# Performance work log

Hardware: AMD Instinct MI355X
Metric: run time of the kernel (lower is better)

Reference implementation:

```python
import jax, jax.numpy as jnp
import numpy as np


def setup_inputs() -> dict:
    key = jax.random.key(0)
    ks = jax.random.split(key, 5)
    B, N, D = 8, 2048, 512
    return {
        "query": jax.random.normal(ks[0], (B, N, D), dtype=jnp.float32),
        "key": jax.random.normal(ks[1], (B, N, D), dtype=jnp.float32),
        "value": jax.random.normal(ks[2], (B, N, D), dtype=jnp.float32),
        "w_k": jax.random.normal(ks[3], (2 * N - 1, D), dtype=jnp.float32),
        "w_v": jax.random.normal(ks[4], (2 * N - 1, D), dtype=jnp.float32),
    }


def reference(query, key, value, w_k, w_v):
    B, N, D = query.shape
    # skew indices: idx[i, j] = (N-1) - i + j  maps (i,j) -> relative distance j-i,
    # distance 0 sits at the middle column (N-1) of the 2N-1 relative table.
    idx = (N - 1) - jnp.arange(N)[:, None] + jnp.arange(N)[None, :]  # [N, N]

    # content scores: [B, N, N]
    base_scores = jnp.einsum("bqd,bkd->bqk", query, key)
    # relative key scores: matmul against full 2N-1 table then skewed gather
    all_rel = jnp.einsum("bqd,rd->bqr", query, w_k)  # [B, N, 2N-1]
    rel_scores = jnp.take_along_axis(
        all_rel, jnp.broadcast_to(idx[None], (B, N, N)), axis=-1
    )
    p_attn = jax.nn.softmax(base_scores + rel_scores, axis=-1)  # [B, N, N]

    # value path: scatter probabilities into skewed [B, N, 2N-1] layout,
    # then one matmul against the relative value table (equivalent to
    # sum_j p[i,j] * w_v[(N-1)-i+j]).
    rows = jnp.arange(N)[:, None]  # [N, 1] broadcast against idx [N, N]
    p_skew = jnp.zeros((B, N, 2 * N - 1), dtype=p_attn.dtype)
    p_skew = p_skew.at[:, rows, idx].set(p_attn)
    rel_out = jnp.einsum("bqr,rd->bqd", p_skew, w_v)

    out = jnp.einsum("bqk,bkd->bqd", p_attn, value) + rel_out
    return out, p_attn
```

## Files before the change

### kernel.cpp

```cpp
#include <hip/hip_runtime.h>


#define SEQN 2048
#define DD   512
#define NB   8
#define WROWS 4095
#define WPAD  4096

typedef float     f32x4 __attribute__((ext_vector_type(4)));
typedef _Float16  h16x4 __attribute__((ext_vector_type(4)));
typedef _Float16  h16x8 __attribute__((ext_vector_type(8)));

__device__ __forceinline__ unsigned swzw(int row, int c4) {
  unsigned b = (unsigned)(row * 64 + c4 * 8);
  return b ^ (((unsigned)row & 6u) << 3);
}
__device__ __forceinline__ unsigned swzr(int row, int kg) {
  unsigned b = (unsigned)(row * 64 + kg * 16);
  return b ^ (((unsigned)row & 6u) << 3);
}

typedef const __attribute__((address_space(1))) unsigned int gu32_t;
typedef __attribute__((address_space(3))) unsigned int lu32_t;
__device__ __forceinline__ void gload_lds16(const void* g, void* l) {
  __builtin_amdgcn_global_load_lds((gu32_t*)g, (lu32_t*)l, 16, 0, 0);
}

template <class P>
__device__ __forceinline__ void stage_tile(const P& prov, char* smem, int buf,
                                           int t, int wave, int l4, int cp) {
  char* lb = smem + buf * 16384;
#pragma unroll
  for (int h = 0; h < 2; h++) {
    int R = wave * 32 + h * 16;
    int row = R + l4;
    int c = cp ^ ((row >> 1) & 3);
    gload_lds16((const char*)prov.a_src(t, row) + c * 16, lb + R * 64);
    gload_lds16((const char*)prov.b_src(t, row) + c * 16, lb + 8192 + R * 64);
  }
}

template <int NT, class P>
__device__ __forceinline__ void gemm_core(const P& prov, char* smem, f32x4 (&acc)[4][4]) {
  const int tid = threadIdx.x;
  const int lane = tid & 63, wave = tid >> 6;
  const int l4 = lane >> 2, cp = lane & 3;
  const int wm = wave >> 1, wn = wave & 1;
  const int r16 = lane & 15, kg = lane >> 4;

  stage_tile(prov, smem, 0, 0, wave, l4, cp);
  asm volatile("s_waitcnt vmcnt(0)" ::: "memory");
  __builtin_amdgcn_s_barrier();
  __builtin_amdgcn_sched_barrier(0);

  int buf = 0;
  for (int t = 0; t < NT; t++) {
    if (t + 1 < NT) stage_tile(prov, smem, buf ^ 1, t + 1, wave, l4, cp);
    char* lb = smem + buf * 16384;
    h16x8 af[4], bf[4];
#pragma unroll
    for (int mf = 0; mf < 4; mf++)
      af[mf] = *(const h16x8*)(lb + swzr(wm * 64 + mf * 16 + r16, kg));
#pragma unroll
    for (int nf = 0; nf < 4; nf++)
      bf[nf] = *(const h16x8*)(lb + 8192 + swzr(wn * 64 + nf * 16 + r16, kg));
#pragma unroll
    for (int mf = 0; mf < 4; mf++)
#pragma unroll
      for (int nf = 0; nf < 4; nf++)
        acc[mf][nf] = __builtin_amdgcn_mfma_f32_16x16x32_f16(af[mf], bf[nf], acc[mf][nf], 0, 0, 0);
    asm volatile("s_waitcnt vmcnt(0)" ::: "memory");
    __builtin_amdgcn_s_barrier();
    __builtin_amdgcn_sched_barrier(0);
    buf ^= 1;
  }
}

struct ProvQK {
  const char *ar, *br;
  __device__ __forceinline__ const void* a_src(int t, int row) const {
    return ar + (size_t)row * 1024 + (size_t)t * 64;
  }
  __device__ __forceinline__ const void* b_src(int t, int row) const {
    return br + (size_t)row * 1024 + (size_t)t * 64;
  }
};
struct ProvRel {
  const char *ar, *wk; int tb;
  __device__ __forceinline__ const void* a_src(int t, int row) const {
    return ar + (size_t)row * 1024 + (size_t)t * 64;
  }
  __device__ __forceinline__ const void* b_src(int t, int row) const {
    int tr = tb + row; if (tr > WROWS - 1) tr = WROWS - 1;
    return wk + (size_t)tr * 1024 + (size_t)t * 64;
  }
};

__global__ __launch_bounds__(256) void cvt_f16_k(const float* __restrict__ in,
                                                 _Float16* __restrict__ out, long n8) {
  for (long i = (long)blockIdx.x * 256 + threadIdx.x; i < n8; i += (long)gridDim.x * 256) {
    f32x4 a = ((const f32x4*)in)[i * 2];
    f32x4 b = ((const f32x4*)in)[i * 2 + 1];
    h16x8 h = {(_Float16)a[0], (_Float16)a[1], (_Float16)a[2], (_Float16)a[3],
               (_Float16)b[0], (_Float16)b[1], (_Float16)b[2], (_Float16)b[3]};
    ((h16x8*)out)[i] = h;
  }
}

__global__ __launch_bounds__(256) void transpose_v_k(const float* __restrict__ v,
                                                     _Float16* __restrict__ vT) {
  __shared__ float tile[32][33];
  const int d0 = blockIdx.x * 32, j0 = blockIdx.y * 32, b = blockIdx.z;
  const int tid = threadIdx.x;
#pragma unroll
  for (int rep = 0; rep < 4; rep++) {
    int idx = rep * 256 + tid;
    int rr = idx >> 5, cc = idx & 31;
    tile[rr][cc] = v[((size_t)(b * SEQN + j0 + rr)) * DD + d0 + cc];
  }
  __syncthreads();
#pragma unroll
  for (int rep = 0; rep < 4; rep++) {
    int idx = rep * 256 + tid;
    int rr = idx >> 5, cc = idx & 31;
    vT[((size_t)(b * DD + d0 + rr)) * SEQN + j0 + cc] = (_Float16)tile[cc][rr];
  }
}

__global__ __launch_bounds__(256) void transpose_wv_k(const float* __restrict__ wv,
                                                      _Float16* __restrict__ wvT) {
  __shared__ float tile[32][33];
  const int d0 = blockIdx.x * 32, r0 = blockIdx.y * 32;
  const int tid = threadIdx.x;
#pragma unroll
  for (int rep = 0; rep < 4; rep++) {
    int idx = rep * 256 + tid;
    int rr = idx >> 5, cc = idx & 31;
    float val = 0.f;
    if (r0 + rr < WROWS) val = wv[(size_t)(r0 + rr) * DD + d0 + cc];
    tile[rr][cc] = val;
  }
  __syncthreads();
#pragma unroll
  for (int rep = 0; rep < 4; rep++) {
    int idx = rep * 256 + tid;
    int rr = idx >> 5, cc = idx & 31;
    wvT[(size_t)(d0 + rr) * WPAD + r0 + cc] = (_Float16)tile[cc][rr];
  }
}

__global__ __launch_bounds__(256) void score_base2_k(const _Float16* __restrict__ qh,
                                                     const _Float16* __restrict__ kh,
                                                     float* __restrict__ S) {
  __shared__ __align__(16) char smem[32768];
  const int j0 = blockIdx.x * 128, i0 = blockIdx.y * 128, b = blockIdx.z;
  const int tid = threadIdx.x, lane = tid & 63, wave = tid >> 6;
  const int wm = wave >> 1, wn = wave & 1, r16 = lane & 15, kg = lane >> 4;

  f32x4 acc[4][4];
#pragma unroll
  for (int mf = 0; mf < 4; mf++)
#pragma unroll
    for (int nf = 0; nf < 4; nf++) acc[mf][nf] = (f32x4){0.f, 0.f, 0.f, 0.f};

  ProvQK prov{(const char*)(qh + (size_t)(b * SEQN + i0) * DD),
              (const char*)(kh + (size_t)(b * SEQN + j0) * DD)};
  gemm_core<16>(prov, smem, acc);

#pragma unroll
  for (int mf = 0; mf < 4; mf++)
#pragma unroll
    for (int nf = 0; nf < 4; nf++)
#pragma unroll
      for (int r = 0; r < 4; r++) {
        int ii = wm * 64 + mf * 16 + kg * 4 + r;
        int jj = wn * 64 + nf * 16 + r16;
        S[(size_t)(b * SEQN + i0 + ii) * SEQN + j0 + jj] = acc[mf][nf][r];
      }
}

__global__ __launch_bounds__(256) void score_rel2_k(const _Float16* __restrict__ qh,
                                                    const _Float16* __restrict__ wkh,
                                                    float* __restrict__ S) {
  __shared__ __align__(16) char smem[32768];
  const int z = blockIdx.x, i0 = blockIdx.y * 128, b = blockIdx.z;
  const int tid = threadIdx.x, lane = tid & 63, wave = tid >> 6;
  const int wm = wave >> 1, wn = wave & 1, r16 = lane & 15, kg = lane >> 4;
  const int tmin = SEQN - 128 - i0;

  f32x4 acc[4][4];
#pragma unroll
  for (int mf = 0; mf < 4; mf++)
#pragma unroll
    for (int nf = 0; nf < 4; nf++) acc[mf][nf] = (f32x4){0.f, 0.f, 0.f, 0.f};

  ProvRel prov{(const char*)(qh + (size_t)(b * SEQN + i0) * DD),
               (const char*)wkh, tmin + z * 128};
  gemm_core<16>(prov, smem, acc);

#pragma unroll
  for (int mf = 0; mf < 4; mf++)
#pragma unroll
    for (int nf = 0; nf < 4; nf++) {
      int bcg = z * 128 + wn * 64 + nf * 16 + r16;
#pragma unroll
      for (int r = 0; r < 4; r++) {
        int ii = wm * 64 + mf * 16 + kg * 4 + r;
        int j = bcg + ii - 127;
        if (bcg <= 2174 && j >= 0 && j < SEQN)
          S[(size_t)(b * SEQN + i0 + ii) * SEQN + j] += acc[mf][nf][r];
      }
    }
}

__global__ __launch_bounds__(256) void softmax_rows_k(float* __restrict__ S) {
  const int wid = threadIdx.x >> 6, lane = threadIdx.x & 63;
  const size_t row = (size_t)blockIdx.x * 4 + wid;
  float* p = S + row * SEQN;
  f32x4 x[8];
  float m = -3.4e38f;
#pragma unroll
  for (int c = 0; c < 8; c++) {
    x[c] = *(const f32x4*)(p + c * 256 + lane * 4);
    m = fmaxf(m, fmaxf(fmaxf(x[c][0], x[c][1]), fmaxf(x[c][2], x[c][3])));
  }
#pragma unroll
  for (int off = 32; off > 0; off >>= 1) m = fmaxf(m, __shfl_xor(m, off));
  float s = 0.f;
#pragma unroll
  for (int c = 0; c < 8; c++)
#pragma unroll
    for (int e = 0; e < 4; e++) {
      x[c][e] = __expf(x[c][e] - m);
      s += x[c][e];
    }
#pragma unroll
  for (int off = 32; off > 0; off >>= 1) s += __shfl_xor(s, off);
  float inv = 1.f / s;
#pragma unroll
  for (int c = 0; c < 8; c++) {
    x[c][0] *= inv; x[c][1] *= inv; x[c][2] *= inv; x[c][3] *= inv;
    *(f32x4*)(p + c * 256 + lane * 4) = x[c];
  }
}

__global__ __launch_bounds__(256) void out_gemm3_k(const float* __restrict__ S,
                                                   const _Float16* __restrict__ vT,
                                                   const _Float16* __restrict__ wvT,
                                                   float* __restrict__ outp) {
  __shared__ __align__(16) char smem[32768];
  const int bid = blockIdx.x;
  const int xcd = bid & 7, rr = bid >> 3;
  const int x = rr & 3, s8 = rr >> 2;
  const int sidx = xcd + 8 * s8;
  const int d0 = x * 128, i0 = (sidx & 15) * 128, b = sidx >> 4;
  const int tid = threadIdx.x, lane = tid & 63, wave = tid >> 6;
  const int wm = wave >> 1, wn = wave & 1, r16 = lane & 15, kg = lane >> 4;
  const int tmin = SEQN - 128 - i0;

  const float*    pb = S  + (size_t)(b * SEQN + i0) * SEQN;
  const _Float16* vb = vT + (size_t)(b * DD + d0) * SEQN;
  const _Float16* wb = wvT + (size_t)d0 * WPAD + tmin;

  f32x4 acc[4][4];
#pragma unroll
  for (int mf = 0; mf < 4; mf++)
#pragma unroll
    for (int nf = 0; nf < 4; nf++) acc[mf][nf] = (f32x4){0.f, 0.f, 0.f, 0.f};

  f32x4 ra[4];
  h16x4 rbv[4];

  auto LOADREGS = [&](int t) {
    if (t < 64) {
      const int k0 = t * 32;
#pragma unroll
      for (int rep = 0; rep < 4; rep++) {
        int f = rep * 256 + tid, row = f >> 3, c4 = f & 7;
        ra[rep]  = *(const f32x4*)(pb + (size_t)row * SEQN + k0 + c4 * 4);
        rbv[rep] = *(const h16x4*)(vb + (size_t)row * SEQN + k0 + c4 * 4);
      }
    } else {
      const int k0 = (t - 64) * 32;
#pragma unroll
      for (int rep = 0; rep < 4; rep++) {
        int f = rep * 256 + tid, row = f >> 3, c4 = f & 7;
        int jb = k0 + c4 * 4 + row - 127;
        const float* pr = pb + (size_t)row * SEQN;
        f32x4 v4;
#pragma unroll
        for (int e = 0; e < 4; e++) {
          int j = jb + e;
          v4[e] = (j >= 0 && j < SEQN) ? pr[j] : 0.f;
        }
        ra[rep]  = v4;
        rbv[rep] = *(const h16x4*)(wb + (size_t)row * WPAD + k0 + c4 * 4);
      }
    }
  };
  auto WRITE = [&](char* lb) {
#pragma unroll
    for (int rep = 0; rep < 4; rep++) {
      int f = rep * 256 + tid, row = f >> 3, c4 = f & 7;
      h16x4 ha = {(_Float16)ra[rep][0], (_Float16)ra[rep][1],
                  (_Float16)ra[rep][2], (_Float16)ra[rep][3]};
      *(h16x4*)(lb + swzw(row, c4)) = ha;
      *(h16x4*)(lb + 8192 + swzw(row, c4)) = rbv[rep];
    }
  };

  LOADREGS(0);
  WRITE(smem);
  LOADREGS(1);
  __syncthreads();

  for (int t = 0; t < 132; t++) {
    char* lb = smem + (t & 1) * 16384;
    if (t + 1 < 132) WRITE(smem + ((t + 1) & 1) * 16384);
    h16x8 af[4], bf[4];
#pragma unroll
    for (int mf = 0; mf < 4; mf++)
      af[mf] = *(const h16x8*)(lb + swzr(wm * 64 + mf * 16 + r16, kg));
#pragma unroll
    for (int nf = 0; nf < 4; nf++)
      bf[nf] = *(const h16x8*)(lb + 8192 + swzr(wn * 64 + nf * 16 + r16, kg));
    if (t + 2 < 132) LOADREGS(t + 2);
#pragma unroll
    for (int mf = 0; mf < 4; mf++)
#pragma unroll
      for (int nf = 0; nf < 4; nf++)
        acc[mf][nf] = __builtin_amdgcn_mfma_f32_16x16x32_f16(af[mf], bf[nf], acc[mf][nf], 0, 0, 0);
    __syncthreads();
  }

#pragma unroll
  for (int mf = 0; mf < 4; mf++)
#pragma unroll
    for (int nf = 0; nf < 4; nf++)
#pragma unroll
      for (int r = 0; r < 4; r++) {
        int ii = wm * 64 + mf * 16 + kg * 4 + r;
        int dd = wn * 64 + nf * 16 + r16;
        outp[(size_t)(b * SEQN + i0 + ii) * DD + d0 + dd] = acc[mf][nf][r];
      }
}

extern "C" void kernel_launch(void* const* d_in, const int* in_sizes, int n_in,
                              void* d_out, int out_size, void* d_ws, size_t ws_size,
                              hipStream_t stream) {
  const float* q  = (const float*)d_in[0];
  const float* k  = (const float*)d_in[1];
  const float* v  = (const float*)d_in[2];
  const float* wk = (const float*)d_in[3];
  const float* wv = (const float*)d_in[4];

  float* outp = (float*)d_out;
  float* S    = outp + (size_t)NB * SEQN * DD;

  const size_t nVT = (size_t)NB * DD * SEQN;
  const size_t nWV = (size_t)DD * WPAD;
  const size_t nQH = (size_t)NB * SEQN * DD;
  _Float16* vT  = (_Float16*)d_ws;
  _Float16* wvT = vT + nVT;
  _Float16* qh  = wvT + nWV;
  _Float16* kh  = qh + nQH;
  _Float16* wkh = kh + nQH;

  cvt_f16_k<<<dim3(2048), 256, 0, stream>>>(q,  qh,  (long)(nQH / 8));
  cvt_f16_k<<<dim3(2048), 256, 0, stream>>>(k,  kh,  (long)(nQH / 8));
  cvt_f16_k<<<dim3(1024), 256, 0, stream>>>(wk, wkh, (long)((size_t)WROWS * DD / 8));
  transpose_v_k <<<dim3(DD / 32, SEQN / 32, NB), 256, 0, stream>>>(v, vT);
  transpose_wv_k<<<dim3(DD / 32, 128),           256, 0, stream>>>(wv, wvT);

  score_base2_k<<<dim3(SEQN / 128, SEQN / 128, NB), 256, 0, stream>>>(qh, kh, S);
  score_rel2_k <<<dim3(17, SEQN / 128, NB),         256, 0, stream>>>(qh, wkh, S);
  softmax_rows_k<<<dim3(NB * SEQN / 4),             256, 0, stream>>>(S);
  out_gemm3_k   <<<dim3(512),                       256, 0, stream>>>(S, vT, wvT, outp);
}
```

Baseline: 414.1 us.

## Triple-buffer score GEMM loads and feed output GEMM with fp16 probabilities

```diff
diff --git a/kernel.cpp b/kernel.cpp
--- a/kernel.cpp
+++ b/kernel.cpp
@@ -41,7 +41,7 @@
 }
 
 template <int NT, class P>
-__device__ __forceinline__ void gemm_core(const P& prov, char* smem, f32x4 (&acc)[4][4]) {
+__device__ __forceinline__ void gemm_core_cnt(const P& prov, char* smem, f32x4 (&acc)[4][4]) {
   const int tid = threadIdx.x;
   const int lane = tid & 63, wave = tid >> 6;
   const int l4 = lane >> 2, cp = lane & 3;
@@ -49,13 +49,13 @@
   const int r16 = lane & 15, kg = lane >> 4;
 
   stage_tile(prov, smem, 0, 0, wave, l4, cp);
-  asm volatile("s_waitcnt vmcnt(0)" ::: "memory");
-  __builtin_amdgcn_s_barrier();
-  __builtin_amdgcn_sched_barrier(0);
+  stage_tile(prov, smem, 1, 1, wave, l4, cp);
+  stage_tile(prov, smem, 2, 2, wave, l4, cp);
 
   int buf = 0;
   for (int t = 0; t < NT; t++) {
-    if (t + 1 < NT) stage_tile(prov, smem, buf ^ 1, t + 1, wave, l4, cp);
+    asm volatile("s_waitcnt vmcnt(8)" ::: "memory");
+    __builtin_amdgcn_s_barrier();
     char* lb = smem + buf * 16384;
     h16x8 af[4], bf[4];
 #pragma unroll
@@ -69,10 +69,11 @@
 #pragma unroll
       for (int nf = 0; nf < 4; nf++)
         acc[mf][nf] = __builtin_amdgcn_mfma_f32_16x16x32_f16(af[mf], bf[nf], acc[mf][nf], 0, 0, 0);
-    asm volatile("s_waitcnt vmcnt(0)" ::: "memory");
+    asm volatile("s_waitcnt lgkmcnt(0)" ::: "memory");
     __builtin_amdgcn_s_barrier();
-    __builtin_amdgcn_sched_barrier(0);
-    buf ^= 1;
+    int nt2 = t + 3; if (nt2 >= NT) nt2 = NT - 1;
+    stage_tile(prov, smem, buf, nt2, wave, l4, cp);
+    buf = (buf == 2) ? 0 : buf + 1;
   }
 }
 
@@ -152,7 +153,7 @@
 __global__ __launch_bounds__(256) void score_base2_k(const _Float16* __restrict__ qh,
                                                      const _Float16* __restrict__ kh,
                                                      float* __restrict__ S) {
-  __shared__ __align__(16) char smem[32768];
+  __shared__ __align__(16) char smem[49152];
   const int j0 = blockIdx.x * 128, i0 = blockIdx.y * 128, b = blockIdx.z;
   const int tid = threadIdx.x, lane = tid & 63, wave = tid >> 6;
   const int wm = wave >> 1, wn = wave & 1, r16 = lane & 15, kg = lane >> 4;
@@ -165,7 +166,7 @@
 
   ProvQK prov{(const char*)(qh + (size_t)(b * SEQN + i0) * DD),
               (const char*)(kh + (size_t)(b * SEQN + j0) * DD)};
-  gemm_core<16>(prov, smem, acc);
+  gemm_core_cnt<16>(prov, smem, acc);
 
 #pragma unroll
   for (int mf = 0; mf < 4; mf++)
@@ -182,7 +183,7 @@
 __global__ __launch_bounds__(256) void score_rel2_k(const _Float16* __restrict__ qh,
                                                     const _Float16* __restrict__ wkh,
                                                     float* __restrict__ S) {
-  __shared__ __align__(16) char smem[32768];
+  __shared__ __align__(16) char smem[49152];
   const int z = blockIdx.x, i0 = blockIdx.y * 128, b = blockIdx.z;
   const int tid = threadIdx.x, lane = tid & 63, wave = tid >> 6;
   const int wm = wave >> 1, wn = wave & 1, r16 = lane & 15, kg = lane >> 4;
@@ -196,7 +197,7 @@
 
   ProvRel prov{(const char*)(qh + (size_t)(b * SEQN + i0) * DD),
                (const char*)wkh, tmin + z * 128};
-  gemm_core<16>(prov, smem, acc);
+  gemm_core_cnt<16>(prov, smem, acc);
 
 #pragma unroll
   for (int mf = 0; mf < 4; mf++)
@@ -213,10 +214,12 @@
     }
 }
 
-__global__ __launch_bounds__(256) void softmax_rows_k(float* __restrict__ S) {
+__global__ __launch_bounds__(256) void softmax_rows_k(float* __restrict__ S,
+                                                      _Float16* __restrict__ ph) {
   const int wid = threadIdx.x >> 6, lane = threadIdx.x & 63;
   const size_t row = (size_t)blockIdx.x * 4 + wid;
   float* p = S + row * SEQN;
+  _Float16* phr = ph + row * SEQN;
   f32x4 x[8];
   float m = -3.4e38f;
 #pragma unroll
@@ -241,10 +244,12 @@
   for (int c = 0; c < 8; c++) {
     x[c][0] *= inv; x[c][1] *= inv; x[c][2] *= inv; x[c][3] *= inv;
     *(f32x4*)(p + c * 256 + lane * 4) = x[c];
-  }
-}
-
-__global__ __launch_bounds__(256) void out_gemm3_k(const float* __restrict__ S,
+    h16x4 h = {(_Float16)x[c][0], (_Float16)x[c][1], (_Float16)x[c][2], (_Float16)x[c][3]};
+    *(h16x4*)(phr + c * 256 + lane * 4) = h;
+  }
+}
+
+__global__ __launch_bounds__(256) void out_gemm4_k(const _Float16* __restrict__ ph,
                                                    const _Float16* __restrict__ vT,
                                                    const _Float16* __restrict__ wvT,
                                                    float* __restrict__ outp) {
@@ -258,7 +263,7 @@
   const int wm = wave >> 1, wn = wave & 1, r16 = lane & 15, kg = lane >> 4;
   const int tmin = SEQN - 128 - i0;
 
-  const float*    pb = S  + (size_t)(b * SEQN + i0) * SEQN;
+  const _Float16* pb = ph + (size_t)(b * SEQN + i0) * SEQN;
   const _Float16* vb = vT + (size_t)(b * DD + d0) * SEQN;
   const _Float16* wb = wvT + (size_t)d0 * WPAD + tmin;
 
@@ -268,8 +273,7 @@
 #pragma unroll
     for (int nf = 0; nf < 4; nf++) acc[mf][nf] = (f32x4){0.f, 0.f, 0.f, 0.f};
 
-  f32x4 ra[4];
-  h16x4 rbv[4];
+  h16x4 rav[4], rbv[4];
 
   auto LOADREGS = [&](int t) {
     if (t < 64) {
@@ -277,7 +281,7 @@
 #pragma unroll
       for (int rep = 0; rep < 4; rep++) {
         int f = rep * 256 + tid, row = f >> 3, c4 = f & 7;
-        ra[rep]  = *(const f32x4*)(pb + (size_t)row * SEQN + k0 + c4 * 4);
+        rav[rep] = *(const h16x4*)(pb + (size_t)row * SEQN + k0 + c4 * 4);
         rbv[rep] = *(const h16x4*)(vb + (size_t)row * SEQN + k0 + c4 * 4);
       }
     } else {
@@ -286,14 +290,14 @@
       for (int rep = 0; rep < 4; rep++) {
         int f = rep * 256 + tid, row = f >> 3, c4 = f & 7;
         int jb = k0 + c4 * 4 + row - 127;
-        const float* pr = pb + (size_t)row * SEQN;
-        f32x4 v4;
+        const _Float16* pr = pb + (size_t)row * SEQN;
+        h16x4 v4;
 #pragma unroll
         for (int e = 0; e < 4; e++) {
           int j = jb + e;
-          v4[e] = (j >= 0 && j < SEQN) ? pr[j] : 0.f;
+          v4[e] = (j >= 0 && j < SEQN) ? pr[j] : (_Float16)0.f;
         }
-        ra[rep]  = v4;
+        rav[rep] = v4;
         rbv[rep] = *(const h16x4*)(wb + (size_t)row * WPAD + k0 + c4 * 4);
       }
     }
@@ -302,9 +306,7 @@
 #pragma unroll
     for (int rep = 0; rep < 4; rep++) {
       int f = rep * 256 + tid, row = f >> 3, c4 = f & 7;
-      h16x4 ha = {(_Float16)ra[rep][0], (_Float16)ra[rep][1],
-                  (_Float16)ra[rep][2], (_Float16)ra[rep][3]};
-      *(h16x4*)(lb + swzw(row, c4)) = ha;
+      *(h16x4*)(lb + swzw(row, c4)) = rav[rep];
       *(h16x4*)(lb + 8192 + swzw(row, c4)) = rbv[rep];
     }
   };
@@ -360,11 +362,13 @@
   const size_t nVT = (size_t)NB * DD * SEQN;
   const size_t nWV = (size_t)DD * WPAD;
   const size_t nQH = (size_t)NB * SEQN * DD;
+  const size_t nWK = 2097152;
   _Float16* vT  = (_Float16*)d_ws;
   _Float16* wvT = vT + nVT;
   _Float16* qh  = wvT + nWV;
   _Float16* kh  = qh + nQH;
   _Float16* wkh = kh + nQH;
+  _Float16* ph  = wkh + nWK;
 
   cvt_f16_k<<<dim3(2048), 256, 0, stream>>>(q,  qh,  (long)(nQH / 8));
   cvt_f16_k<<<dim3(2048), 256, 0, stream>>>(k,  kh,  (long)(nQH / 8));
@@ -372,8 +376,8 @@
   transpose_v_k <<<dim3(DD / 32, SEQN / 32, NB), 256, 0, stream>>>(v, vT);
   transpose_wv_k<<<dim3(DD / 32, 128),           256, 0, stream>>>(wv, wvT);
 
-  score_base2_k<<<dim3(SEQN / 128, SEQN / 128, NB), 256, 0, stream>>>(qh, kh, S);
-  score_rel2_k <<<dim3(17, SEQN / 128, NB),         256, 0, stream>>>(qh, wkh, S);
-  softmax_rows_k<<<dim3(NB * SEQN / 4),             256, 0, stream>>>(S);
-  out_gemm3_k   <<<dim3(512),                       256, 0, stream>>>(S, vT, wvT, outp);
-}
+  score_base2_k <<<dim3(SEQN / 128, SEQN / 128, NB), 256, 0, stream>>>(qh, kh, S);
+  score_rel2_k  <<<dim3(17, SEQN / 128, NB),         256, 0, stream>>>(qh, wkh, S);
+  softmax_rows_k<<<dim3(NB * SEQN / 4),              256, 0, stream>>>(S, ph);
+  out_gemm4_k   <<<dim3(512),                        256, 0, stream>>>(ph, vT, wvT, outp);
+}
```

Result: slower. 434.6 us (+4.9%).
